# Optimization experiments

Hardware: AMD Instinct MI355X
Metric: run time of the kernel (lower is better)

Reference implementation:

```python
import jax, jax.numpy as jnp
import numpy as np

M, N, F = 512, 128, 512  # molecules, atoms per molecule, feature dim
HID, OUT = F // 4, 1


def setup_inputs() -> dict:
    key = jax.random.key(0)
    k1, k2, k3 = jax.random.split(key, 3)
    h = jax.random.normal(k1, (M, N, F), dtype=jnp.float32)
    W1 = jax.random.normal(k2, (F, HID), dtype=jnp.float32) * (1.0 / np.sqrt(F))
    b1 = jnp.zeros((HID,), dtype=jnp.float32)
    W2 = jax.random.normal(k3, (HID, OUT), dtype=jnp.float32) * (1.0 / np.sqrt(HID))
    b2 = jnp.zeros((OUT,), dtype=jnp.float32)
    return {"h": h, "W1": W1, "b1": b1, "W2": W2, "b2": b2}


def reference(h, W1, b1, W2, b2):
    # method == 'weighted_summation'
    # gate MLP: Linear -> ReLU -> Linear -> Sigmoid, per atom
    w = jax.nn.sigmoid(jax.nn.relu(h @ W1 + b1) @ W2 + b2)  # [M, N, OUT]
    # per-molecule weighted sum over atoms: mm(w_h.T, h) for each molecule,
    # concatenated along dim 0 -> [M*OUT, F] (OUT=1 -> [M, F])
    out = jnp.einsum('mno,mnf->mof', w, h)  # [M, OUT, F]
    return out.reshape(M * OUT, F)
```

## Files before the change

### kernel.cpp

```cpp
#include <hip/hip_runtime.h>
#include <hip/hip_bf16.h>


typedef unsigned short u16;
typedef unsigned int u32;
typedef __bf16 bf16x8 __attribute__((ext_vector_type(8)));
typedef float f32x4 __attribute__((ext_vector_type(4)));
typedef float f32x2 __attribute__((ext_vector_type(2)));
typedef u32 u32x4 __attribute__((ext_vector_type(4)));

#define M_MOL 512
#define N_ATOM 128
#define F_DIM 512
#define HID_DIM 128
#define ABLK 64
#define NBLK (M_MOL * 2)

static __device__ __forceinline__ u16 f2bf(float x) {
  u32 u = __float_as_uint(x);
  u32 r = (u + 0x7fffu + ((u >> 16) & 1u)) >> 16;
  return (u16)r;
}
static __device__ __forceinline__ bf16x8 pack8(u32x4 a, u32x4 b) {
  u32x4 r;
  r[0] = (a[0] >> 16) | (a[1] & 0xffff0000u);
  r[1] = (a[2] >> 16) | (a[3] & 0xffff0000u);
  r[2] = (b[0] >> 16) | (b[1] & 0xffff0000u);
  r[3] = (b[2] >> 16) | (b[3] & 0xffff0000u);
  return __builtin_bit_cast(bf16x8, r);
}

__global__ __launch_bounds__(256) void transpose_w1(const float* __restrict__ W1,
                                                    u16* __restrict__ W1T) {
  __shared__ float tile[64][65];
  const int k0 = blockIdx.x * 64;
  const int n0 = blockIdx.y * 64;
  const int t = threadIdx.x;
  #pragma unroll
  for (int i = 0; i < 16; ++i) {
    const int lin = i * 256 + t;
    const int lr = lin >> 6, lc = lin & 63;
    tile[lc][lr] = W1[(size_t)(k0 + lr) * HID_DIM + (n0 + lc)];
  }
  __syncthreads();
  #pragma unroll
  for (int i = 0; i < 16; ++i) {
    const int lin = i * 256 + t;
    const int wr = lin >> 6, wc = lin & 63;
    W1T[(size_t)(n0 + wr) * F_DIM + (k0 + wc)] = f2bf(tile[wr][wc]);
  }
}

__global__ __launch_bounds__(256, 4) void pool_partial(
    const float* __restrict__ h, const u16* __restrict__ W1T,
    const float* __restrict__ b1, const float* __restrict__ W2,
    const float* __restrict__ b2, float* __restrict__ part) {
  __shared__ union SM {
    u16 bt[HID_DIM * 32];
    float red[4][F_DIM];
  } sm;
  __shared__ float w_s[ABLK];

  const int blk = blockIdx.x;
  const int tid = threadIdx.x;
  const int wv = tid >> 6;
  const int lane = tid & 63;
  const int quad = lane >> 4;
  const int cl = lane & 15;

  const float* hb = h + (size_t)blk * ABLK * F_DIM;

  const float* arow = hb + (size_t)(wv * 16 + cl) * F_DIM;
  const int kb = quad * 8;

  const int srow = tid >> 1;
  const int scol = (tid & 1) * 16;
  const u16* sg = W1T + (size_t)srow * F_DIM + scol;
  u16* sl = sm.bt + srow * 32 + scol;

  f32x4 acc[8];
  #pragma unroll
  for (int t = 0; t < 8; ++t) acc[t] = (f32x4){0.f, 0.f, 0.f, 0.f};

  u32x4 st0 = *(const u32x4*)sg;
  u32x4 st1 = *(const u32x4*)(sg + 8);
  u32x4 a_lo = *(const u32x4*)(arow + kb);
  u32x4 a_hi = *(const u32x4*)(arow + kb + 4);

  #pragma unroll 2
  for (int ks = 0; ks < 16; ++ks) {
    __syncthreads();
    *(u32x4*)sl = st0;
    *(u32x4*)(sl + 8) = st1;
    __syncthreads();
    if (ks < 15) {
      st0 = *(const u32x4*)(sg + (ks + 1) * 32);
      st1 = *(const u32x4*)(sg + (ks + 1) * 32 + 8);
    }
    bf16x8 afr = pack8(a_lo, a_hi);
    if (ks < 15) {
      a_lo = *(const u32x4*)(arow + (ks + 1) * 32 + kb);
      a_hi = *(const u32x4*)(arow + (ks + 1) * 32 + kb + 4);
    }
    #pragma unroll
    for (int t = 0; t < 8; ++t) {
      bf16x8 bfr = *(const bf16x8*)(sm.bt + (t * 16 + cl) * 32 + kb);
      acc[t] = __builtin_amdgcn_mfma_f32_16x16x32_bf16(afr, bfr, acc[t], 0, 0, 0);
    }
  }

  float psum[4] = {0.f, 0.f, 0.f, 0.f};
  #pragma unroll
  for (int t = 0; t < 8; ++t) {
    const int hid = t * 16 + cl;
    const float b1v = b1[hid];
    const float w2v = W2[hid];
    #pragma unroll
    for (int r = 0; r < 4; ++r) {
      float tv = fmaxf(acc[t][r] + b1v, 0.f);
      psum[r] = fmaf(tv, w2v, psum[r]);
    }
  }
  #pragma unroll
  for (int off = 1; off < 16; off <<= 1)
    #pragma unroll
    for (int r = 0; r < 4; ++r)
      psum[r] += __shfl_xor(psum[r], off, 64);
  if (cl == 0) {
    const float b2v = b2[0];
    #pragma unroll
    for (int r = 0; r < 4; ++r)
      w_s[wv * 16 + quad * 4 + r] = 1.f / (1.f + __expf(-(psum[r] + b2v)));
  }
  __syncthreads();

  float facc[8] = {0.f, 0.f, 0.f, 0.f, 0.f, 0.f, 0.f, 0.f};
  const int f0 = lane * 8;
  const float* hrow = hb + (size_t)(wv * 16) * F_DIM + f0;
  #pragma unroll 4
  for (int i = 0; i < 16; ++i) {
    const float wn = w_s[wv * 16 + i];
    f32x4 h0 = *(const f32x4*)(hrow + (size_t)i * F_DIM);
    f32x4 h1 = *(const f32x4*)(hrow + (size_t)i * F_DIM + 4);
    #pragma unroll
    for (int j = 0; j < 4; ++j) {
      facc[j]     = fmaf(wn, h0[j], facc[j]);
      facc[j + 4] = fmaf(wn, h1[j], facc[j + 4]);
    }
  }
  #pragma unroll
  for (int j = 0; j < 8; ++j) sm.red[wv][f0 + j] = facc[j];
  __syncthreads();

  {
    const int f = tid * 2;
    f32x2 o;
    o[0] = sm.red[0][f] + sm.red[1][f] + sm.red[2][f] + sm.red[3][f];
    o[1] = sm.red[0][f + 1] + sm.red[1][f + 1] + sm.red[2][f + 1] + sm.red[3][f + 1];
    *(f32x2*)(part + (size_t)blk * F_DIM + f) = o;
  }
}

__global__ __launch_bounds__(256) void reduce_out(const float* __restrict__ part,
                                                  float* __restrict__ out) {
  const int m = blockIdx.x;
  const int f = threadIdx.x * 2;
  f32x2 a = *(const f32x2*)(part + (size_t)(2 * m) * F_DIM + f);
  f32x2 b = *(const f32x2*)(part + (size_t)(2 * m + 1) * F_DIM + f);
  f32x2 o;
  o[0] = a[0] + b[0];
  o[1] = a[1] + b[1];
  *(f32x2*)(out + (size_t)m * F_DIM + f) = o;
}

extern "C" void kernel_launch(void* const* d_in, const int* in_sizes, int n_in,
                              void* d_out, int out_size, void* d_ws, size_t ws_size,
                              hipStream_t stream) {
  const float* h  = (const float*)d_in[0];
  const float* W1 = (const float*)d_in[1];
  const float* b1 = (const float*)d_in[2];
  const float* W2 = (const float*)d_in[3];
  const float* b2 = (const float*)d_in[4];
  float* out = (float*)d_out;

  u16* W1T = (u16*)d_ws;
  float* part = (float*)((char*)d_ws + HID_DIM * F_DIM * sizeof(u16));

  transpose_w1<<<dim3(8, 2), 256, 0, stream>>>(W1, W1T);
  pool_partial<<<NBLK, 256, 0, stream>>>(h, W1T, b1, W2, b2, part);
  reduce_out<<<M_MOL, 256, 0, stream>>>(part, out);
}
```

Before: 223.6 us.

## Stage whole h tile as bf16 in LDS and reuse it for pooling

Each block now loads its 64x512 slice of h once, converts it to bf16 and stores it swizzled in shared memory. That copy feeds both the MFMA gate GEMM and the weighted atom sum, so h is no longer read from global memory a second time. W1 is pre-tiled into k-major 32-column panels and double-buffered in LDS, which leaves one barrier per k-step. In exchange the pooling sum now uses bf16-rounded h instead of fp32, and the larger LDS footprint lowers occupancy to 2 blocks per CU.

```diff
diff --git a/kernel.cpp b/kernel.cpp
--- a/kernel.cpp
+++ b/kernel.cpp
@@ -31,7 +31,7 @@
 }
 
 __global__ __launch_bounds__(256) void transpose_w1(const float* __restrict__ W1,
-                                                    u16* __restrict__ W1T) {
+                                                    u16* __restrict__ W1Tt) {
   __shared__ float tile[64][65];
   const int k0 = blockIdx.x * 64;
   const int n0 = blockIdx.y * 64;
@@ -47,19 +47,25 @@
   for (int i = 0; i < 16; ++i) {
     const int lin = i * 256 + t;
     const int wr = lin >> 6, wc = lin & 63;
-    W1T[(size_t)(n0 + wr) * F_DIM + (k0 + wc)] = f2bf(tile[wr][wc]);
-  }
-}
-
-__global__ __launch_bounds__(256, 4) void pool_partial(
-    const float* __restrict__ h, const u16* __restrict__ W1T,
+    const int k = k0 + wc;
+    W1Tt[(size_t)(k >> 5) * (HID_DIM * 32) + (size_t)(n0 + wr) * 32 + (k & 31)] =
+        f2bf(tile[wr][wc]);
+  }
+}
+
+__global__ __launch_bounds__(256, 2) void pool_partial(
+    const float* __restrict__ h, const u16* __restrict__ W1Tt,
     const float* __restrict__ b1, const float* __restrict__ W2,
     const float* __restrict__ b2, float* __restrict__ part) {
-  __shared__ union SM {
-    u16 bt[HID_DIM * 32];
-    float red[4][F_DIM];
+  __shared__ u16 As[ABLK * F_DIM];
+  __shared__ union U {
+    u16 bt[2][HID_DIM * 32];
+    struct {
+      float w_s[ABLK];
+      float _pad[2048 - ABLK];
+      float red[4][F_DIM];
+    } s;
   } sm;
-  __shared__ float w_s[ABLK];
 
   const int blk = blockIdx.x;
   const int tid = threadIdx.x;
@@ -68,44 +74,63 @@
   const int quad = lane >> 4;
   const int cl = lane & 15;
 
-  const float* hb = h + (size_t)blk * ABLK * F_DIM;
-
-  const float* arow = hb + (size_t)(wv * 16 + cl) * F_DIM;
-  const int kb = quad * 8;
-
-  const int srow = tid >> 1;
-  const int scol = (tid & 1) * 16;
-  const u16* sg = W1T + (size_t)srow * F_DIM + scol;
-  u16* sl = sm.bt + srow * 32 + scol;
+  {
+    const u32x4* hg = (const u32x4*)(h + (size_t)blk * ABLK * F_DIM);
+    #pragma unroll
+    for (int i = 0; i < 16; ++i) {
+      const int u = i * 256 + tid;
+      const int row = u >> 6;
+      const int c = u & 63;
+      u32x4 lo = hg[2 * u];
+      u32x4 hi = hg[2 * u + 1];
+      const int phys = (c & ~7) | ((c ^ row) & 7);
+      *(bf16x8*)(As + row * F_DIM + phys * 8) = pack8(lo, hi);
+    }
+  }
+
+  const u16* wg = W1Tt + tid * 16;
+  const int brow = tid >> 1;
+  const int bc0 = 2 * (tid & 1);
+  u16* bw0 = sm.bt[0] + brow * 32;
+  u16* bw1 = sm.bt[1] + brow * 32;
+  const int bphysA = (bc0 ^ (brow & 3)) * 8;
+  const int bphysB = ((bc0 + 1) ^ (brow & 3)) * 8;
+  {
+    u32x4 v0 = *(const u32x4*)wg;
+    u32x4 v1 = *(const u32x4*)(wg + 8);
+    *(u32x4*)(bw0 + bphysA) = v0;
+    *(u32x4*)(bw0 + bphysB) = v1;
+  }
+  __syncthreads();
 
   f32x4 acc[8];
   #pragma unroll
   for (int t = 0; t < 8; ++t) acc[t] = (f32x4){0.f, 0.f, 0.f, 0.f};
 
-  u32x4 st0 = *(const u32x4*)sg;
-  u32x4 st1 = *(const u32x4*)(sg + 8);
-  u32x4 a_lo = *(const u32x4*)(arow + kb);
-  u32x4 a_hi = *(const u32x4*)(arow + kb + 4);
-
-  #pragma unroll 2
+  const int ar = wv * 16 + cl;
+  const u16* aBase = As + ar * F_DIM;
+  const int bq = (quad ^ (cl & 3)) * 8;
+
   for (int ks = 0; ks < 16; ++ks) {
-    __syncthreads();
-    *(u32x4*)sl = st0;
-    *(u32x4*)(sl + 8) = st1;
-    __syncthreads();
+    u32x4 v0, v1;
     if (ks < 15) {
-      st0 = *(const u32x4*)(sg + (ks + 1) * 32);
-      st1 = *(const u32x4*)(sg + (ks + 1) * 32 + 8);
-    }
-    bf16x8 afr = pack8(a_lo, a_hi);
+      v0 = *(const u32x4*)(wg + (ks + 1) * (HID_DIM * 32));
+      v1 = *(const u32x4*)(wg + (ks + 1) * (HID_DIM * 32) + 8);
+    }
+    const int c = ks * 4 + quad;
+    const int aphys = (c & ~7) | ((c ^ ar) & 7);
+    bf16x8 afr = *(const bf16x8*)(aBase + aphys * 8);
+    const u16* btb = sm.bt[ks & 1];
+    #pragma unroll
+    for (int t = 0; t < 8; ++t) {
+      bf16x8 bfr = *(const bf16x8*)(btb + (t * 16 + cl) * 32 + bq);
+      acc[t] = __builtin_amdgcn_mfma_f32_16x16x32_bf16(afr, bfr, acc[t], 0, 0, 0);
+    }
     if (ks < 15) {
-      a_lo = *(const u32x4*)(arow + (ks + 1) * 32 + kb);
-      a_hi = *(const u32x4*)(arow + (ks + 1) * 32 + kb + 4);
-    }
-    #pragma unroll
-    for (int t = 0; t < 8; ++t) {
-      bf16x8 bfr = *(const bf16x8*)(sm.bt + (t * 16 + cl) * 32 + kb);
-      acc[t] = __builtin_amdgcn_mfma_f32_16x16x32_bf16(afr, bfr, acc[t], 0, 0, 0);
+      u16* bw = (ks & 1) ? bw0 : bw1;
+      *(u32x4*)(bw + bphysA) = v0;
+      *(u32x4*)(bw + bphysB) = v1;
+      __syncthreads();
     }
   }
 
@@ -130,33 +155,33 @@
     const float b2v = b2[0];
     #pragma unroll
     for (int r = 0; r < 4; ++r)
-      w_s[wv * 16 + quad * 4 + r] = 1.f / (1.f + __expf(-(psum[r] + b2v)));
+      sm.s.w_s[wv * 16 + quad * 4 + r] = 1.f / (1.f + __expf(-(psum[r] + b2v)));
   }
   __syncthreads();
 
   float facc[8] = {0.f, 0.f, 0.f, 0.f, 0.f, 0.f, 0.f, 0.f};
-  const int f0 = lane * 8;
-  const float* hrow = hb + (size_t)(wv * 16) * F_DIM + f0;
   #pragma unroll 4
   for (int i = 0; i < 16; ++i) {
-    const float wn = w_s[wv * 16 + i];
-    f32x4 h0 = *(const f32x4*)(hrow + (size_t)i * F_DIM);
-    f32x4 h1 = *(const f32x4*)(hrow + (size_t)i * F_DIM + 4);
+    const int row = wv * 16 + i;
+    const float wn = sm.s.w_s[row];
+    const int phys = (lane & ~7) | ((lane ^ row) & 7);
+    bf16x8 hv = *(const bf16x8*)(As + row * F_DIM + phys * 8);
+    u32x4 uv = __builtin_bit_cast(u32x4, hv);
     #pragma unroll
     for (int j = 0; j < 4; ++j) {
-      facc[j]     = fmaf(wn, h0[j], facc[j]);
-      facc[j + 4] = fmaf(wn, h1[j], facc[j + 4]);
-    }
-  }
-  #pragma unroll
-  for (int j = 0; j < 8; ++j) sm.red[wv][f0 + j] = facc[j];
+      facc[2 * j]     = fmaf(wn, __uint_as_float(uv[j] << 16), facc[2 * j]);
+      facc[2 * j + 1] = fmaf(wn, __uint_as_float(uv[j] & 0xffff0000u), facc[2 * j + 1]);
+    }
+  }
+  #pragma unroll
+  for (int j = 0; j < 8; ++j) sm.s.red[wv][lane * 8 + j] = facc[j];
   __syncthreads();
 
   {
     const int f = tid * 2;
     f32x2 o;
-    o[0] = sm.red[0][f] + sm.red[1][f] + sm.red[2][f] + sm.red[3][f];
-    o[1] = sm.red[0][f + 1] + sm.red[1][f + 1] + sm.red[2][f + 1] + sm.red[3][f + 1];
+    o[0] = sm.s.red[0][f] + sm.s.red[1][f] + sm.s.red[2][f] + sm.s.red[3][f];
+    o[1] = sm.s.red[0][f + 1] + sm.s.red[1][f + 1] + sm.s.red[2][f + 1] + sm.s.red[3][f + 1];
     *(f32x2*)(part + (size_t)blk * F_DIM + f) = o;
   }
 }
@@ -183,10 +208,10 @@
   const float* b2 = (const float*)d_in[4];
   float* out = (float*)d_out;
 
-  u16* W1T = (u16*)d_ws;
-  float* part = (float*)((char*)d_ws + HID_DIM * F_DIM * sizeof(u16));
-
-  transpose_w1<<<dim3(8, 2), 256, 0, stream>>>(W1, W1T);
-  pool_partial<<<NBLK, 256, 0, stream>>>(h, W1T, b1, W2, b2, part);
+  u16* W1Tt = (u16*)d_ws;
+  float* part = (float*)((char*)d_ws + (size_t)HID_DIM * F_DIM * sizeof(u16));
+
+  transpose_w1<<<dim3(8, 2), 256, 0, stream>>>(W1, W1Tt);
+  pool_partial<<<NBLK, 256, 0, stream>>>(h, W1Tt, b1, W2, b2, part);
   reduce_out<<<M_MOL, 256, 0, stream>>>(part, out);
 }
```

Result: faster. 214.1 us (-4.2%).
